# Performance work log

Hardware: AMD Instinct MI355X
Metric: run time of the kernel (lower is better)

Reference implementation:

```python
import jax, jax.numpy as jnp
import numpy as np

N_HEAD = 16

def rel_shift(x):
    # x: (qlen, klen, B, n). Pad one zero column at front of klen axis,
    # reinterpret as (klen+1, qlen, B, n), drop first row, reshape back.
    qlen, klen, b, n = x.shape
    x_pad = jnp.pad(x, ((0, 0), (1, 0), (0, 0), (0, 0)))
    x_pad = x_pad.reshape(klen + 1, qlen, b, n)
    return x_pad[1:].reshape(qlen, klen, b, n)

def setup_inputs() -> dict:
    key = jax.random.key(0)
    ks = jax.random.split(key, 9)
    qlen = klen = 1024
    B = 4
    d_model = 1024
    d_head = d_model // N_HEAD
    q = jax.random.normal(ks[0], (qlen, B, d_model), jnp.float32)
    K = jax.random.normal(ks[1], (klen, B, d_model), jnp.float32)
    V = jax.random.normal(ks[2], (klen, B, d_model), jnp.float32)
    mask = jax.random.bernoulli(ks[3], 0.1, (1, klen, B, 1))
    r = jax.random.normal(ks[4], (klen, d_model), jnp.float32)
    u = jax.random.normal(ks[5], (N_HEAD, d_head), jnp.float32) * 0.02
    v = jax.random.normal(ks[6], (N_HEAD, d_head), jnp.float32) * 0.02
    Wr = jax.random.normal(ks[7], (d_model, d_model), jnp.float32) / np.sqrt(d_model)
    br = jax.random.normal(ks[8], (d_model,), jnp.float32) * 0.02
    return {"q": q, "K": K, "V": V, "mask": mask, "r": r, "u": u, "v": v, "Wr": Wr, "br": br}

def reference(q, K, V, mask, r, u, v, Wr, br):
    qlen, bsz, d_model = q.shape
    klen = K.shape[0]
    d_head = d_model // N_HEAD
    qh = q.reshape(qlen, bsz, N_HEAD, d_head)
    Kh = K.reshape(klen, bsz, N_HEAD, d_head)
    Vh = V.reshape(klen, bsz, N_HEAD, d_head)
    rh = (r @ Wr.T + br).reshape(klen, N_HEAD, d_head)  # r_net projection
    AC = jnp.einsum('ibnd,jbnd->ijbn', qh + u, Kh)
    BD = rel_shift(jnp.einsum('ibnd,jnd->ijbn', qh + v, rh))
    score = (AC + BD) / jnp.sqrt(jnp.asarray(d_head, q.dtype))
    # mask (1,klen,B,1) broadcasts over qlen and heads (torch repeats over heads)
    score = jnp.where(mask, jnp.asarray(-1e9, score.dtype), score)
    weight = jax.nn.softmax(score, axis=1)
    out = jnp.einsum('ijbn,jbnd->ibnd', weight, Vh).reshape(qlen, bsz, d_model)
    return out, weight.mean(axis=-1)
```

## Files before the change

kernel.cpp:

```cpp
#include <hip/hip_runtime.h>
#include <hip/hip_fp16.h>
#include <stdint.h>


#define L 1024
#define BATCH 4
#define NH 16
#define DH 64
#define DM 1024
#define TI 16
#define NJT 16
#define BDP_ST 1032
#define SCALE 0.125f

typedef __attribute__((ext_vector_type(8))) short short8;
typedef __attribute__((ext_vector_type(4))) float f32x4;

static __device__ __forceinline__ unsigned short f2bf(float f) {
    union { float f; unsigned int u; } x; x.f = f;
    return (unsigned short)((x.u + 0x7fffu + ((x.u >> 16) & 1u)) >> 16);
}
static __device__ __forceinline__ float bf2f(unsigned short h) {
    union { unsigned int u; float f; } x; x.u = ((unsigned int)h) << 16;
    return x.f;
}
static __device__ __forceinline__ unsigned short f2h(float f) {
    __half h = __float2half(f);
    union { __half h; unsigned short s; } x; x.h = h; return x.s;
}
static __device__ __forceinline__ float h2f(unsigned short s) {
    union { __half h; unsigned short s; } x; x.s = s; return __half2float(x.h);
}
static __device__ __forceinline__ unsigned short* usp(void* base, int byteoff) {
    return (unsigned short*)((char*)base + byteoff);
}
static __device__ __forceinline__ short8 ld8(const void* base, int byteoff) {
    return *(const short8*)((const char*)base + byteoff);
}
#define SW128(row, colByte) ((((row) * 128) + (colByte)) ^ (((row) & 7) << 4))

__global__ __launch_bounds__(256) void rh_gemm_kernel(
    const float* __restrict__ r, const float* __restrict__ Wr,
    const float* __restrict__ br, float* __restrict__ rhf,
    unsigned short* __restrict__ rhb, int bfmode)
{
    __shared__ float As[16][65];
    __shared__ float Bs[16][65];
    const int j0 = blockIdx.x * 64;
    const int m0 = blockIdx.y * 64;
    const int tid = threadIdx.x;
    const int ty = tid >> 4, tx = tid & 15;
    float acc[4][4] = {};

    for (int k0 = 0; k0 < DM; k0 += 16) {
        const int row = tid >> 2, c4 = (tid & 3) << 2;
        float4 av = *(const float4*)(r  + (size_t)(j0 + row) * DM + k0 + c4);
        float4 bv = *(const float4*)(Wr + (size_t)(m0 + row) * DM + k0 + c4);
        __syncthreads();
        As[c4 + 0][row] = av.x; As[c4 + 1][row] = av.y;
        As[c4 + 2][row] = av.z; As[c4 + 3][row] = av.w;
        Bs[c4 + 0][row] = bv.x; Bs[c4 + 1][row] = bv.y;
        Bs[c4 + 2][row] = bv.z; Bs[c4 + 3][row] = bv.w;
        __syncthreads();
#pragma unroll
        for (int k = 0; k < 16; ++k) {
            float a[4], bb[4];
#pragma unroll
            for (int t = 0; t < 4; ++t) { a[t] = As[k][ty * 4 + t]; bb[t] = Bs[k][tx * 4 + t]; }
#pragma unroll
            for (int ii = 0; ii < 4; ++ii)
#pragma unroll
                for (int jj = 0; jj < 4; ++jj)
                    acc[ii][jj] = fmaf(a[ii], bb[jj], acc[ii][jj]);
        }
    }
#pragma unroll
    for (int ii = 0; ii < 4; ++ii) {
        const int row = j0 + ty * 4 + ii;
#pragma unroll
        for (int jj = 0; jj < 4; ++jj) {
            const int col = m0 + tx * 4 + jj;
            const float val = acc[ii][jj] + br[col];
            if (bfmode)
                rhb[(((size_t)(col >> 6)) * L + row) * DH + (col & 63)] = f2bf(val);
            else
                rhf[(size_t)row * DM + col] = val;
        }
    }
}

__global__ __launch_bounds__(256) void prepass_kernel(
    const float* __restrict__ Kg, const float* __restrict__ Vg,
    unsigned short* __restrict__ Kbf, unsigned short* __restrict__ Vtb)
{
    __shared__ unsigned short tile[64][80];
    const int j0 = blockIdx.x * 64;
    const int b = blockIdx.y, n = blockIdx.z;
    const int bn = b * NH + n;
    const int tid = threadIdx.x;

    for (int idx = tid; idx < 64 * 16; idx += 256) {
        const int jr = idx >> 4, s4 = (idx & 15) * 4;
        const size_t src = ((size_t)(j0 + jr) * BATCH + b) * DM + n * DH + s4;
        float4 kv = *(const float4*)(Kg + src);
        ushort4 o;
        o.x = f2bf(kv.x); o.y = f2bf(kv.y); o.z = f2bf(kv.z); o.w = f2bf(kv.w);
        *(ushort4*)(Kbf + ((size_t)bn * L + j0 + jr) * DH + s4) = o;
        float4 vv4 = *(const float4*)(Vg + src);
        tile[s4 + 0][jr] = f2bf(vv4.x); tile[s4 + 1][jr] = f2bf(vv4.y);
        tile[s4 + 2][jr] = f2bf(vv4.z); tile[s4 + 3][jr] = f2bf(vv4.w);
    }
    __syncthreads();
    for (int idx = tid; idx < 64 * 8; idx += 256) {
        const int d = idx >> 3, p8 = (idx & 7) * 8;
        short8 o = *(const short8*)&tile[d][p8];
        *(short8*)(Vtb + ((size_t)bn * DH + d) * L + j0 + p8) = o;
    }
}

__global__ __launch_bounds__(256) void wm_reduce_kernel(
    const unsigned short* __restrict__ W_ws, float* __restrict__ wm_out)
{
    const int gi = blockIdx.x;
    const int b  = blockIdx.y;
    const int j0 = threadIdx.x * 4;
    float acc0 = 0.f, acc1 = 0.f, acc2 = 0.f, acc3 = 0.f;
#pragma unroll
    for (int n = 0; n < NH; ++n) {
        ushort4 wv = *(const ushort4*)(W_ws + (((size_t)(b * NH + n) * L + gi) * L) + j0);
        acc0 += bf2f(wv.x); acc1 += bf2f(wv.y);
        acc2 += bf2f(wv.z); acc3 += bf2f(wv.w);
    }
    const size_t o = ((size_t)gi * L + j0) * BATCH + b;
    wm_out[o]             = acc0 * (1.f / 16.f);
    wm_out[o + BATCH]     = acc1 * (1.f / 16.f);
    wm_out[o + 2 * BATCH] = acc2 * (1.f / 16.f);
    wm_out[o + 3 * BATCH] = acc3 * (1.f / 16.f);
}

template<int MODE, int PLAIN>
__global__ __launch_bounds__(256, 2) void attn_kernel(
    const float* __restrict__ q,
    const void* __restrict__ Kp, const void* __restrict__ Vp,
    const unsigned char* __restrict__ maskp,
    const float* __restrict__ uu, const float* __restrict__ vvp,
    const void* __restrict__ rhp,
    float* __restrict__ out, float* __restrict__ wm_out,
    unsigned short* __restrict__ W_ws)
{
    __shared__ unsigned short QU[16 * 64];
    __shared__ unsigned short QV[17 * 64];
    __shared__ unsigned short KR[(MODE == 1) ? 64 * 64 : 8];
    __shared__ unsigned short VT[(MODE == 1) ? 64 * 64 : 8];
    __shared__ unsigned short BDp[17 * BDP_ST];
    __shared__ unsigned short Wt[16 * 64];
    __shared__ unsigned char mblk[L];
    __shared__ float denomP[4][16];
    __shared__ float rdenom[16];
    __shared__ int mflags;

    const int i0 = blockIdx.x * TI;
    const int b  = blockIdx.y;
    const int n  = blockIdx.z;
    const int bn = b * NH + n;
    const int tid = threadIdx.x;
    const int w = tid >> 6, lane = tid & 63, lr = lane & 15, lg = lane >> 4;

    const unsigned short* Kbf = (const unsigned short*)Kp;
    const unsigned short* Vtb = (const unsigned short*)Vp;
    const unsigned short* rhb = (const unsigned short*)rhp;
    const float* Kg  = (const float*)Kp;
    const float* Vg  = (const float*)Vp;
    const float* rhf = (const float*)rhp;

    if (tid == 0) mflags = 0;
    __syncthreads();
    {
        int local = 0;
        for (int ww = tid; ww < 1024; ww += 256) {
            const unsigned int word = ((const unsigned int*)maskp)[ww];
            if (word == 0x3f800000u) local |= 1;
            else if (word & 0xffffff00u) local |= 2;
        }
        if (local) atomicOr(&mflags, local);
    }
    __syncthreads();
    {
        const int mtype = (mflags & 1) ? 2 : ((mflags & 2) ? 1 : 0);
        for (int j = tid; j < L; j += 256) {
            bool mv;
            if (mtype == 2)      mv = ((const float*)maskp)[j * BATCH + b] != 0.f;
            else if (mtype == 1) mv = maskp[j * BATCH + b] != 0;
            else                 mv = ((const int*)maskp)[j * BATCH + b] != 0;
            mblk[j] = mv ? 1 : 0;
        }
    }
    for (int idx = tid; idx < 17 * 64; idx += 256) {
        const int row = idx >> 6, d = idx & 63;
        const int gi = i0 + row;
        const float qval = (gi < L) ? q[((size_t)gi * BATCH + b) * DM + n * DH + d] : 0.f;
        *usp(QV, SW128(row, d * 2)) = f2bf(qval + vvp[n * DH + d]);
        if (row < 16) *usp(QU, SW128(row, d * 2)) = f2bf(qval + uu[n * DH + d]);
    }
    __syncthreads();

    for (int ct = 0; ct < 16; ++ct) {
        const int c0 = ct * 64;
        if constexpr (MODE == 1) {
            __syncthreads();
            for (int idx = tid; idx < 64 * 16; idx += 256) {
                const int cr = idx >> 4, d4 = (idx & 15) * 4;
                float4 rv = *(const float4*)(rhf + (size_t)(c0 + cr) * DM + n * DH + d4);
                unsigned short* p = usp(KR, SW128(cr, d4 * 2));
                p[0] = f2bf(rv.x); p[1] = f2bf(rv.y); p[2] = f2bf(rv.z); p[3] = f2bf(rv.w);
            }
            __syncthreads();
        }
        const int ccol = w * 16 + lr;
        f32x4 acc = {0.f, 0.f, 0.f, 0.f};
#pragma unroll
        for (int kh = 0; kh < 2; ++kh) {
            short8 a = ld8(QV, SW128(lr, (kh * 32 + lg * 8) * 2));
            short8 bb;
            if constexpr (MODE == 0)
                bb = *(const short8*)(rhb + ((size_t)n * L + c0 + ccol) * DH + kh * 32 + lg * 8);
            else
                bb = ld8(KR, SW128(ccol, (kh * 32 + lg * 8) * 2));
            acc = __builtin_amdgcn_mfma_f32_16x16x32_bf16(a, bb, acc, 0, 0, 0);
        }
#pragma unroll
        for (int r2 = 0; r2 < 4; ++r2)
            BDp[(lg * 4 + r2) * BDP_ST + c0 + ccol] = f2h(acc[r2]);
        {
            const int col = tid >> 2, kq = (tid & 3) * 16;
            float s16 = 0.f;
#pragma unroll
            for (int kk = 0; kk < 16; kk += 8) {
                short8 qa = ld8(QV, SW128(16, (kq + kk) * 2));
                short8 ra;
                if constexpr (MODE == 0)
                    ra = *(const short8*)(rhb + ((size_t)n * L + c0 + col) * DH + kq + kk);
                else
                    ra = ld8(KR, SW128(col, (kq + kk) * 2));
#pragma unroll
                for (int e = 0; e < 8; ++e)
                    s16 = fmaf(bf2f((unsigned short)qa[e]), bf2f((unsigned short)ra[e]), s16);
            }
            s16 += __shfl_xor(s16, 1);
            s16 += __shfl_xor(s16, 2);
            if ((tid & 3) == 0) BDp[16 * BDP_ST + c0 + col] = f2h(s16);
        }
    }
    __syncthreads();

    f32x4 pv = {0.f, 0.f, 0.f, 0.f};
    float dl[4] = {0.f, 0.f, 0.f, 0.f};
    float tmp[4][NJT];
    const int jloc = w * 16 + lr;
#pragma unroll
    for (int jt = 0; jt < NJT; ++jt) {
        const int j0 = jt * 64;
        const int gj = j0 + jloc;
        if constexpr (MODE == 1) {
            for (int idx = tid; idx < 64 * 16; idx += 256) {
                const int jr = idx >> 4, d4 = (idx & 15) * 4;
                const size_t src = ((size_t)(j0 + jr) * BATCH + b) * DM + n * DH + d4;
                float4 kv = *(const float4*)(Kg + src);
                unsigned short* p = usp(KR, SW128(jr, d4 * 2));
                p[0] = f2bf(kv.x); p[1] = f2bf(kv.y); p[2] = f2bf(kv.z); p[3] = f2bf(kv.w);
                float4 vv4 = *(const float4*)(Vg + src);
                *usp(VT, SW128(d4 + 0, jr * 2)) = f2bf(vv4.x);
                *usp(VT, SW128(d4 + 1, jr * 2)) = f2bf(vv4.y);
                *usp(VT, SW128(d4 + 2, jr * 2)) = f2bf(vv4.z);
                *usp(VT, SW128(d4 + 3, jr * 2)) = f2bf(vv4.w);
            }
            __syncthreads();
        }
        f32x4 acc = {0.f, 0.f, 0.f, 0.f};
#pragma unroll
        for (int kh = 0; kh < 2; ++kh) {
            short8 a = ld8(QU, SW128(lr, (kh * 32 + lg * 8) * 2));
            short8 bb;
            if constexpr (MODE == 0)
                bb = *(const short8*)(Kbf + ((size_t)bn * L + gj) * DH + kh * 32 + lg * 8);
            else
                bb = ld8(KR, SW128(jloc, (kh * 32 + lg * 8) * 2));
            acc = __builtin_amdgcn_mfma_f32_16x16x32_bf16(a, bb, acc, 0, 0, 0);
        }
        const bool msk = mblk[gj] != 0;
#pragma unroll
        for (int r2 = 0; r2 < 4; ++r2) {
            const int il = lg * 4 + r2;
            const int gi = i0 + il;
            const int t = gj - gi;
            float bd = 0.f;
            if (t != 1) {
                const int c = (t <= 0) ? (L - 1 + t) : (t - 2);
                bd = h2f(BDp[(il + (t >= 1 ? 1 : 0)) * BDP_ST + c]);
            }
            float s = (acc[r2] + bd) * SCALE;
            if (msk) s = -1e9f;
            const float wgt = __expf(fminf(s, 80.f));
            dl[r2] += wgt;
            tmp[r2][jt] = wgt;
            *usp(Wt, SW128(il, jloc * 2)) = f2bf(wgt);
        }
        __syncthreads();
#pragma unroll
        for (int kh = 0; kh < 2; ++kh) {
            short8 a = ld8(Wt, SW128(lr, (kh * 32 + lg * 8) * 2));
            short8 bb;
            if constexpr (MODE == 0)
                bb = *(const short8*)(Vtb + ((size_t)bn * DH + jloc) * L + j0 + kh * 32 + lg * 8);
            else
                bb = ld8(VT, SW128(jloc, (kh * 32 + lg * 8) * 2));
            pv = __builtin_amdgcn_mfma_f32_16x16x32_bf16(a, bb, pv, 0, 0, 0);
        }
        __syncthreads();
    }

#pragma unroll
    for (int r2 = 0; r2 < 4; ++r2) {
        float d = dl[r2];
        d += __shfl_xor(d, 1); d += __shfl_xor(d, 2);
        d += __shfl_xor(d, 4); d += __shfl_xor(d, 8);
        if (lr == 0) denomP[w][lg * 4 + r2] = d;
    }
    __syncthreads();
    if (tid < 16)
        rdenom[tid] = 1.f / (denomP[0][tid] + denomP[1][tid] + denomP[2][tid] + denomP[3][tid]);
    __syncthreads();

#pragma unroll
    for (int r2 = 0; r2 < 4; ++r2) {
        const int il = lg * 4 + r2;
        out[((size_t)(i0 + il) * BATCH + b) * DM + n * DH + w * 16 + lr] = pv[r2] * rdenom[il];
    }

    if constexpr (PLAIN == 1) {
#pragma unroll
        for (int r2 = 0; r2 < 4; ++r2) {
            const int il = lg * 4 + r2;
            const float rs = rdenom[il];
            const size_t rowo = ((size_t)bn * L + i0 + il) * L;
#pragma unroll
            for (int jt = 0; jt < NJT; ++jt)
                W_ws[rowo + jt * 64 + jloc] = f2bf(tmp[r2][jt] * rs);
        }
    } else {
#pragma unroll
        for (int r2 = 0; r2 < 4; ++r2) {
            const int il = lg * 4 + r2;
            const float rs = rdenom[il] * (1.f / 16.f);
#pragma unroll
            for (int jt = 0; jt < NJT; ++jt)
                atomicAdd(wm_out + ((size_t)(i0 + il) * L + jt * 64 + jloc) * BATCH + b,
                          tmp[r2][jt] * rs);
        }
    }
}

extern "C" void kernel_launch(void* const* d_in, const int* in_sizes, int n_in,
                              void* d_out, int out_size, void* d_ws, size_t ws_size,
                              hipStream_t stream)
{
    (void)in_sizes; (void)n_in; (void)out_size;
    const float* q   = (const float*)d_in[0];
    const float* K   = (const float*)d_in[1];
    const float* V   = (const float*)d_in[2];
    const unsigned char* mask = (const unsigned char*)d_in[3];
    const float* r   = (const float*)d_in[4];
    const float* u   = (const float*)d_in[5];
    const float* v   = (const float*)d_in[6];
    const float* Wr  = (const float*)d_in[7];
    const float* br  = (const float*)d_in[8];

    float* out = (float*)d_out;
    float* wm  = out + (size_t)L * BATCH * DM;

    const size_t kvbytes = (size_t)BATCH * NH * L * DH * 2;
    const size_t rhbytes = (size_t)NH * L * DH * 2;
    const size_t wmbytes = (size_t)BATCH * NH * L * L * 2;

    if (ws_size >= 2 * kvbytes + rhbytes + wmbytes) {
        unsigned short* Kbf = (unsigned short*)d_ws;
        unsigned short* Vtb = Kbf + kvbytes / 2;
        unsigned short* rhb = Vtb + kvbytes / 2;
        unsigned short* Wws = rhb + rhbytes / 2;
        rh_gemm_kernel<<<dim3(16, 16), 256, 0, stream>>>(r, Wr, br, nullptr, rhb, 1);
        prepass_kernel<<<dim3(16, 4, 16), 256, 0, stream>>>(K, V, Kbf, Vtb);
        attn_kernel<0, 1><<<dim3(64, 4, 16), 256, 0, stream>>>(
            q, Kbf, Vtb, mask, u, v, rhb, out, wm, Wws);
        wm_reduce_kernel<<<dim3(L, BATCH), 256, 0, stream>>>(Wws, wm);
    } else if (ws_size >= 2 * kvbytes + rhbytes) {
        hipMemsetAsync(wm, 0, (size_t)L * L * BATCH * sizeof(float), stream);
        unsigned short* Kbf = (unsigned short*)d_ws;
        unsigned short* Vtb = Kbf + kvbytes / 2;
        unsigned short* rhb = Vtb + kvbytes / 2;
        rh_gemm_kernel<<<dim3(16, 16), 256, 0, stream>>>(r, Wr, br, nullptr, rhb, 1);
        prepass_kernel<<<dim3(16, 4, 16), 256, 0, stream>>>(K, V, Kbf, Vtb);
        attn_kernel<0, 0><<<dim3(64, 4, 16), 256, 0, stream>>>(
            q, Kbf, Vtb, mask, u, v, rhb, out, wm, nullptr);
    } else {
        hipMemsetAsync(wm, 0, (size_t)L * L * BATCH * sizeof(float), stream);
        float* rhf = (float*)d_ws;
        rh_gemm_kernel<<<dim3(16, 16), 256, 0, stream>>>(r, Wr, br, rhf, nullptr, 0);
        attn_kernel<1, 0><<<dim3(64, 4, 16), 256, 0, stream>>>(
            q, K, V, mask, u, v, rhf, out, wm, nullptr);
    }
}
```

Before: 356.6 us.

## Rewrite attention path with MFMA r-projection, exp2 softmax, and streamed weight writes

Replaces the scalar FP32 r_net GEMM with a bf16 MFMA kernel. The main attention kernel is reworked: Q+u/Q+v operands are kept in registers and pre-scaled by log2(e)/sqrt(d), and K/R/V fragments are prefetched from global memory with double buffering. Softmax uses exp2 without max subtraction, and per-wave PV accumulation runs over 256-key slabs without block-wide syncs. Unnormalized bf16 weights go straight to the workspace, and the reduction kernel applies per-row reciprocal denominators. Occupancy is raised to 3 blocks per CU; the trade-offs are bf16 rounding of r_net and the loss of overflow safety from skipping max subtraction.

```diff
diff --git a/kernel.cpp b/kernel.cpp
--- a/kernel.cpp
+++ b/kernel.cpp
@@ -12,6 +12,7 @@
 #define NJT 16
 #define BDP_ST 1032
 #define SCALE 0.125f
+#define CS 0.18033688011112042f
 
 typedef __attribute__((ext_vector_type(8))) short short8;
 typedef __attribute__((ext_vector_type(4))) float f32x4;
@@ -37,12 +38,63 @@
 static __device__ __forceinline__ short8 ld8(const void* base, int byteoff) {
     return *(const short8*)((const char*)base + byteoff);
 }
+static __device__ __forceinline__ float fexp2(float x) {
+#if __has_builtin(__builtin_amdgcn_exp2f)
+    return __builtin_amdgcn_exp2f(x);
+#else
+    return __expf(x * 0.6931471805599453f);
+#endif
+}
 #define SW128(row, colByte) ((((row) * 128) + (colByte)) ^ (((row) & 7) << 4))
+
+__global__ __launch_bounds__(256) void rh_gemm_mfma(
+    const float* __restrict__ r, const float* __restrict__ Wr,
+    const float* __restrict__ br, unsigned short* __restrict__ rhb)
+{
+    __shared__ unsigned short rT[64 * 64];
+    __shared__ unsigned short wT[64 * 64];
+    const int c0 = blockIdx.x * 64, m0 = blockIdx.y * 64;
+    const int tid = threadIdx.x;
+    const int w = tid >> 6, lane = tid & 63, lr = lane & 15, lg = lane >> 4;
+    f32x4 acc[4] = {};
+
+    for (int kt = 0; kt < 16; ++kt) {
+        const int k0 = kt * 64;
+        __syncthreads();
+        const int row = tid >> 2, cb = (tid & 3) * 16;
+#pragma unroll
+        for (int q4 = 0; q4 < 4; ++q4) {
+            float4 rv = *(const float4*)(r + (size_t)(c0 + row) * DM + k0 + cb + q4 * 4);
+            unsigned short* p = usp(rT, SW128(row, (cb + q4 * 4) * 2));
+            p[0] = f2bf(rv.x); p[1] = f2bf(rv.y); p[2] = f2bf(rv.z); p[3] = f2bf(rv.w);
+            float4 wv = *(const float4*)(Wr + (size_t)(m0 + row) * DM + k0 + cb + q4 * 4);
+            unsigned short* pw = usp(wT, SW128(row, (cb + q4 * 4) * 2));
+            pw[0] = f2bf(wv.x); pw[1] = f2bf(wv.y); pw[2] = f2bf(wv.z); pw[3] = f2bf(wv.w);
+        }
+        __syncthreads();
+#pragma unroll
+        for (int mch = 0; mch < 4; ++mch)
+#pragma unroll
+            for (int kh = 0; kh < 2; ++kh) {
+                short8 a  = ld8(rT, SW128(w * 16 + lr,   (kh * 32 + lg * 8) * 2));
+                short8 bb = ld8(wT, SW128(mch * 16 + lr, (kh * 32 + lg * 8) * 2));
+                acc[mch] = __builtin_amdgcn_mfma_f32_16x16x32_bf16(a, bb, acc[mch], 0, 0, 0);
+            }
+    }
+#pragma unroll
+    for (int mch = 0; mch < 4; ++mch)
+#pragma unroll
+        for (int r2 = 0; r2 < 4; ++r2) {
+            const int c = c0 + w * 16 + lg * 4 + r2;
+            const int d = mch * 16 + lr;
+            const float val = acc[mch][r2] + br[m0 + d];
+            rhb[((size_t)blockIdx.y * L + c) * DH + d] = f2bf(val);
+        }
+}
 
 __global__ __launch_bounds__(256) void rh_gemm_kernel(
     const float* __restrict__ r, const float* __restrict__ Wr,
-    const float* __restrict__ br, float* __restrict__ rhf,
-    unsigned short* __restrict__ rhb, int bfmode)
+    const float* __restrict__ br, float* __restrict__ rhf)
 {
     __shared__ float As[16][65];
     __shared__ float Bs[16][65];
@@ -80,11 +132,7 @@
 #pragma unroll
         for (int jj = 0; jj < 4; ++jj) {
             const int col = m0 + tx * 4 + jj;
-            const float val = acc[ii][jj] + br[col];
-            if (bfmode)
-                rhb[(((size_t)(col >> 6)) * L + row) * DH + (col & 63)] = f2bf(val);
-            else
-                rhf[(size_t)row * DM + col] = val;
+            rhf[(size_t)row * DM + col] = acc[ii][jj] + br[col];
         }
     }
 }
@@ -119,41 +167,39 @@
 }
 
 __global__ __launch_bounds__(256) void wm_reduce_kernel(
-    const unsigned short* __restrict__ W_ws, float* __restrict__ wm_out)
+    const unsigned short* __restrict__ W_ws, const float* __restrict__ rdeng,
+    float* __restrict__ wm_out)
 {
     const int gi = blockIdx.x;
     const int b  = blockIdx.y;
     const int j0 = threadIdx.x * 4;
-    float acc0 = 0.f, acc1 = 0.f, acc2 = 0.f, acc3 = 0.f;
+    float a0 = 0.f, a1 = 0.f, a2 = 0.f, a3 = 0.f;
 #pragma unroll
     for (int n = 0; n < NH; ++n) {
-        ushort4 wv = *(const ushort4*)(W_ws + (((size_t)(b * NH + n) * L + gi) * L) + j0);
-        acc0 += bf2f(wv.x); acc1 += bf2f(wv.y);
-        acc2 += bf2f(wv.z); acc3 += bf2f(wv.w);
+        const int bn = b * NH + n;
+        const float rd = rdeng[((size_t)bn << 10) + gi];
+        ushort4 wv = *(const ushort4*)(W_ws + ((size_t)bn * L + gi) * L + j0);
+        a0 += bf2f(wv.x) * rd; a1 += bf2f(wv.y) * rd;
+        a2 += bf2f(wv.z) * rd; a3 += bf2f(wv.w) * rd;
     }
     const size_t o = ((size_t)gi * L + j0) * BATCH + b;
-    wm_out[o]             = acc0 * (1.f / 16.f);
-    wm_out[o + BATCH]     = acc1 * (1.f / 16.f);
-    wm_out[o + 2 * BATCH] = acc2 * (1.f / 16.f);
-    wm_out[o + 3 * BATCH] = acc3 * (1.f / 16.f);
-}
-
-template<int MODE, int PLAIN>
-__global__ __launch_bounds__(256, 2) void attn_kernel(
+    wm_out[o]             = a0;
+    wm_out[o + BATCH]     = a1;
+    wm_out[o + 2 * BATCH] = a2;
+    wm_out[o + 3 * BATCH] = a3;
+}
+
+__global__ __launch_bounds__(256, 3) void attn_fused(
     const float* __restrict__ q,
-    const void* __restrict__ Kp, const void* __restrict__ Vp,
+    const unsigned short* __restrict__ Kbf, const unsigned short* __restrict__ Vtb,
     const unsigned char* __restrict__ maskp,
     const float* __restrict__ uu, const float* __restrict__ vvp,
-    const void* __restrict__ rhp,
-    float* __restrict__ out, float* __restrict__ wm_out,
-    unsigned short* __restrict__ W_ws)
+    const unsigned short* __restrict__ rhb,
+    float* __restrict__ out, unsigned short* __restrict__ W_ws,
+    float* __restrict__ rdeng)
 {
-    __shared__ unsigned short QU[16 * 64];
-    __shared__ unsigned short QV[17 * 64];
-    __shared__ unsigned short KR[(MODE == 1) ? 64 * 64 : 8];
-    __shared__ unsigned short VT[(MODE == 1) ? 64 * 64 : 8];
-    __shared__ unsigned short BDp[17 * BDP_ST];
-    __shared__ unsigned short Wt[16 * 64];
+    __shared__ __align__(16) unsigned short BDp[17 * BDP_ST];
+    __shared__ __align__(16) unsigned short Wt[4][2][16 * 64];
     __shared__ unsigned char mblk[L];
     __shared__ float denomP[4][16];
     __shared__ float rdenom[16];
@@ -165,13 +211,6 @@
     const int bn = b * NH + n;
     const int tid = threadIdx.x;
     const int w = tid >> 6, lane = tid & 63, lr = lane & 15, lg = lane >> 4;
-
-    const unsigned short* Kbf = (const unsigned short*)Kp;
-    const unsigned short* Vtb = (const unsigned short*)Vp;
-    const unsigned short* rhb = (const unsigned short*)rhp;
-    const float* Kg  = (const float*)Kp;
-    const float* Vg  = (const float*)Vp;
-    const float* rhf = (const float*)rhp;
 
     if (tid == 0) mflags = 0;
     __syncthreads();
@@ -195,17 +234,264 @@
             mblk[j] = mv ? 1 : 0;
         }
     }
+    if (tid < 17 * 8) {
+        const int row = tid >> 3, cp = tid & 7;
+        BDp[row * BDP_ST + 1024 + cp] = 0;
+    }
+
+    const float* qrow = q + ((size_t)(i0 + lr) * BATCH + b) * DM + n * DH;
+    const float* urow = uu + n * DH;
+    const float* vrow = vvp + n * DH;
+    short8 qu_a[2], qv_a[2];
+#pragma unroll
+    for (int kh = 0; kh < 2; ++kh) {
+        const int kb = kh * 32 + lg * 8;
+        float4 qa = *(const float4*)(qrow + kb), qb = *(const float4*)(qrow + kb + 4);
+        float4 ua = *(const float4*)(urow + kb), ub = *(const float4*)(urow + kb + 4);
+        float4 va = *(const float4*)(vrow + kb), vb = *(const float4*)(vrow + kb + 4);
+        short8 su, sv;
+        su[0] = (short)f2bf((qa.x + ua.x) * CS); su[1] = (short)f2bf((qa.y + ua.y) * CS);
+        su[2] = (short)f2bf((qa.z + ua.z) * CS); su[3] = (short)f2bf((qa.w + ua.w) * CS);
+        su[4] = (short)f2bf((qb.x + ub.x) * CS); su[5] = (short)f2bf((qb.y + ub.y) * CS);
+        su[6] = (short)f2bf((qb.z + ub.z) * CS); su[7] = (short)f2bf((qb.w + ub.w) * CS);
+        sv[0] = (short)f2bf((qa.x + va.x) * CS); sv[1] = (short)f2bf((qa.y + va.y) * CS);
+        sv[2] = (short)f2bf((qa.z + va.z) * CS); sv[3] = (short)f2bf((qa.w + va.w) * CS);
+        sv[4] = (short)f2bf((qb.x + vb.x) * CS); sv[5] = (short)f2bf((qb.y + vb.y) * CS);
+        sv[6] = (short)f2bf((qb.z + vb.z) * CS); sv[7] = (short)f2bf((qb.w + vb.w) * CS);
+        qu_a[kh] = su; qv_a[kh] = sv;
+    }
+    float qv16[16];
+    {
+        const int kq = (tid & 3) * 16;
+        if (i0 + 16 < L) {
+            const float* q16 = q + ((size_t)(i0 + 16) * BATCH + b) * DM + n * DH;
+#pragma unroll
+            for (int e4 = 0; e4 < 4; ++e4) {
+                float4 qa = *(const float4*)(q16 + kq + e4 * 4);
+                float4 va = *(const float4*)(vrow + kq + e4 * 4);
+                qv16[e4 * 4 + 0] = (qa.x + va.x) * CS; qv16[e4 * 4 + 1] = (qa.y + va.y) * CS;
+                qv16[e4 * 4 + 2] = (qa.z + va.z) * CS; qv16[e4 * 4 + 3] = (qa.w + va.w) * CS;
+            }
+        } else {
+#pragma unroll
+            for (int e = 0; e < 16; ++e) qv16[e] = 0.f;
+        }
+    }
+
+    {
+        const unsigned short* rpane = rhb + (size_t)n * L * DH;
+        const int ccol = w * 16 + lr;
+        short8 rb[2][2];
+#pragma unroll
+        for (int kh = 0; kh < 2; ++kh)
+            rb[0][kh] = *(const short8*)(rpane + (size_t)ccol * DH + kh * 32 + lg * 8);
+        const int col16 = tid >> 2;
+        const int kq = (tid & 3) * 16;
+#pragma unroll
+        for (int ct = 0; ct < 16; ++ct) {
+            const int c0 = ct * 64;
+            const int cur = ct & 1;
+            if (ct + 1 < 16) {
+#pragma unroll
+                for (int kh = 0; kh < 2; ++kh)
+                    rb[cur ^ 1][kh] = *(const short8*)(rpane + (size_t)((ct + 1) * 64 + ccol) * DH + kh * 32 + lg * 8);
+            }
+            f32x4 acc = {0.f, 0.f, 0.f, 0.f};
+#pragma unroll
+            for (int kh = 0; kh < 2; ++kh)
+                acc = __builtin_amdgcn_mfma_f32_16x16x32_bf16(qv_a[kh], rb[cur][kh], acc, 0, 0, 0);
+#pragma unroll
+            for (int r2 = 0; r2 < 4; ++r2)
+                BDp[(lg * 4 + r2) * BDP_ST + c0 + ccol] = f2h(acc[r2]);
+            {
+                short8 ra0 = *(const short8*)(rpane + (size_t)(c0 + col16) * DH + kq);
+                short8 ra1 = *(const short8*)(rpane + (size_t)(c0 + col16) * DH + kq + 8);
+                float s16 = 0.f;
+#pragma unroll
+                for (int e = 0; e < 8; ++e) {
+                    s16 = fmaf(qv16[e],     bf2f((unsigned short)ra0[e]), s16);
+                    s16 = fmaf(qv16[e + 8], bf2f((unsigned short)ra1[e]), s16);
+                }
+                s16 += __shfl_xor(s16, 1);
+                s16 += __shfl_xor(s16, 2);
+                if ((tid & 3) == 0) BDp[16 * BDP_ST + c0 + col16] = f2h(s16);
+            }
+        }
+    }
+    __syncthreads();
+
+    const unsigned short* Kpane = Kbf + (size_t)bn * L * DH;
+    const unsigned short* Vpane = Vtb + (size_t)bn * DH * L;
+    const int jwbase = w * 256;
+    f32x4 pv[4] = {};
+    float dl[4] = {0.f, 0.f, 0.f, 0.f};
+    int ilb[4];
+    size_t wsrow[4];
+#pragma unroll
+    for (int r2 = 0; r2 < 4; ++r2) {
+        ilb[r2] = (lg * 4 + r2) * BDP_ST;
+        wsrow[r2] = ((size_t)bn * L + i0 + lg * 4 + r2) * L;
+    }
+    short8 kf[2][2];
+#pragma unroll
+    for (int kh = 0; kh < 2; ++kh)
+        kf[0][kh] = *(const short8*)(Kpane + (size_t)(jwbase + lr) * DH + kh * 32 + lg * 8);
+
+#pragma unroll 1
+    for (int sub = 0; sub < 4; ++sub) {
+        const int jbase = jwbase + sub * 64;
+        unsigned short* WtW = &Wt[w][sub & 1][0];
+        short8 vfr[8];
+#pragma unroll
+        for (int dch = 0; dch < 4; ++dch)
+#pragma unroll
+            for (int kh = 0; kh < 2; ++kh)
+                vfr[dch * 2 + kh] = *(const short8*)(Vpane + (size_t)(dch * 16 + lr) * L + jbase + kh * 32 + lg * 8);
+#pragma unroll
+        for (int c4 = 0; c4 < 4; ++c4) {
+            const int chunk = sub * 4 + c4;
+            const int cur = c4 & 1;
+            if (chunk + 1 < 16) {
+#pragma unroll
+                for (int kh = 0; kh < 2; ++kh)
+                    kf[cur ^ 1][kh] = *(const short8*)(Kpane + (size_t)(jwbase + (chunk + 1) * 16 + lr) * DH + kh * 32 + lg * 8);
+            }
+            f32x4 acc = {0.f, 0.f, 0.f, 0.f};
+#pragma unroll
+            for (int kh = 0; kh < 2; ++kh)
+                acc = __builtin_amdgcn_mfma_f32_16x16x32_bf16(qu_a[kh], kf[cur][kh], acc, 0, 0, 0);
+            const int gj = jbase + c4 * 16 + lr;
+            const float mo = mblk[gj] ? -1e9f : 0.f;
+            const int ebase = gj - i0 - lg * 4;
+#pragma unroll
+            for (int r2 = 0; r2 < 4; ++r2) {
+                const int e = ebase - r2;
+                const int addr = ilb[r2] + e + ((e <= 0) ? 1023 : 1030);
+                const float bd = h2f(BDp[addr]);
+                float s = fminf(acc[r2] + bd + mo, 126.f);
+                const float wg = fexp2(s);
+                dl[r2] += wg;
+                const unsigned short wb = f2bf(wg);
+                *usp(WtW, SW128(lg * 4 + r2, (c4 * 16 + lr) * 2)) = wb;
+                W_ws[wsrow[r2] + gj] = wb;
+            }
+        }
+#pragma unroll
+        for (int dch = 0; dch < 4; ++dch)
+#pragma unroll
+            for (int kh = 0; kh < 2; ++kh) {
+                short8 a = ld8(WtW, SW128(lr, (kh * 32 + lg * 8) * 2));
+                pv[dch] = __builtin_amdgcn_mfma_f32_16x16x32_bf16(a, vfr[dch * 2 + kh], pv[dch], 0, 0, 0);
+            }
+    }
+
+#pragma unroll
+    for (int r2 = 0; r2 < 4; ++r2) {
+        float d = dl[r2];
+        d += __shfl_xor(d, 1); d += __shfl_xor(d, 2);
+        d += __shfl_xor(d, 4); d += __shfl_xor(d, 8);
+        if (lr == 0) denomP[w][lg * 4 + r2] = d;
+    }
+    {
+        float* pvw = (float*)&Wt[w][0][0];
+#pragma unroll
+        for (int dch = 0; dch < 4; ++dch)
+#pragma unroll
+            for (int r2 = 0; r2 < 4; ++r2)
+                pvw[(lg * 4 + r2) * 64 + dch * 16 + lr] = pv[dch][r2];
+    }
+    __syncthreads();
+    if (tid < 16) {
+        const float dn = denomP[0][tid] + denomP[1][tid] + denomP[2][tid] + denomP[3][tid];
+        rdenom[tid] = 1.f / dn;
+        rdeng[((size_t)bn << 10) + i0 + tid] = 1.f / (dn * 16.f);
+    }
+    __syncthreads();
+
+    {
+        const float* pvwAll = (const float*)&Wt[0][0][0];
+        const int il = tid >> 4, d0 = (tid & 15) * 4;
+        float4 o = *(const float4*)(pvwAll + 0 * 1024 + il * 64 + d0);
+        float4 o1 = *(const float4*)(pvwAll + 1 * 1024 + il * 64 + d0);
+        float4 o2 = *(const float4*)(pvwAll + 2 * 1024 + il * 64 + d0);
+        float4 o3 = *(const float4*)(pvwAll + 3 * 1024 + il * 64 + d0);
+        const float rs = rdenom[il];
+        o.x = (o.x + o1.x + o2.x + o3.x) * rs;
+        o.y = (o.y + o1.y + o2.y + o3.y) * rs;
+        o.z = (o.z + o1.z + o2.z + o3.z) * rs;
+        o.w = (o.w + o1.w + o2.w + o3.w) * rs;
+        *(float4*)(out + ((size_t)(i0 + il) * BATCH + b) * DM + n * DH + d0) = o;
+    }
+}
+
+template<int MODE>
+__global__ __launch_bounds__(256, 2) void attn_legacy(
+    const float* __restrict__ q,
+    const void* __restrict__ Kp, const void* __restrict__ Vp,
+    const unsigned char* __restrict__ maskp,
+    const float* __restrict__ uu, const float* __restrict__ vvp,
+    const void* __restrict__ rhp,
+    float* __restrict__ out, float* __restrict__ wm_out)
+{
+    __shared__ unsigned short QU[16 * 64];
+    __shared__ unsigned short QV[17 * 64];
+    __shared__ unsigned short KR[(MODE == 1) ? 64 * 64 : 8];
+    __shared__ unsigned short VT[(MODE == 1) ? 64 * 64 : 8];
+    __shared__ unsigned short BDp[17 * BDP_ST];
+    __shared__ unsigned short Wt[2][16 * 64];
+    __shared__ unsigned char mblk[L];
+    __shared__ float denomP[4][16];
+    __shared__ float rdenom[16];
+    __shared__ int mflags;
+
+    const int i0 = blockIdx.x * TI;
+    const int b  = blockIdx.y;
+    const int n  = blockIdx.z;
+    const int bn = b * NH + n;
+    const int tid = threadIdx.x;
+    const int w = tid >> 6, lane = tid & 63, lr = lane & 15, lg = lane >> 4;
+
+    const unsigned short* Kbf = (const unsigned short*)Kp;
+    const unsigned short* Vtb = (const unsigned short*)Vp;
+    const unsigned short* rhb = (const unsigned short*)rhp;
+    const float* Kg  = (const float*)Kp;
+    const float* Vg  = (const float*)Vp;
+    const float* rhf = (const float*)rhp;
+
+    if (tid == 0) mflags = 0;
+    __syncthreads();
+    {
+        int local = 0;
+        for (int ww = tid; ww < 1024; ww += 256) {
+            const unsigned int word = ((const unsigned int*)maskp)[ww];
+            if (word == 0x3f800000u) local |= 1;
+            else if (word & 0xffffff00u) local |= 2;
+        }
+        if (local) atomicOr(&mflags, local);
+    }
+    __syncthreads();
+    {
+        const int mtype = (mflags & 1) ? 2 : ((mflags & 2) ? 1 : 0);
+        for (int j = tid; j < L; j += 256) {
+            bool mv;
+            if (mtype == 2)      mv = ((const float*)maskp)[j * BATCH + b] != 0.f;
+            else if (mtype == 1) mv = maskp[j * BATCH + b] != 0;
+            else                 mv = ((const int*)maskp)[j * BATCH + b] != 0;
+            mblk[j] = mv ? 1 : 0;
+        }
+    }
     for (int idx = tid; idx < 17 * 64; idx += 256) {
         const int row = idx >> 6, d = idx & 63;
         const int gi = i0 + row;
         const float qval = (gi < L) ? q[((size_t)gi * BATCH + b) * DM + n * DH + d] : 0.f;
-        *usp(QV, SW128(row, d * 2)) = f2bf(qval + vvp[n * DH + d]);
-        if (row < 16) *usp(QU, SW128(row, d * 2)) = f2bf(qval + uu[n * DH + d]);
+        *usp(QV, SW128(row, d * 2)) = f2bf((qval + vvp[n * DH + d]) * SCALE);
+        if (row < 16) *usp(QU, SW128(row, d * 2)) = f2bf((qval + uu[n * DH + d]) * SCALE);
     }
     __syncthreads();
 
     for (int ct = 0; ct < 16; ++ct) {
         const int c0 = ct * 64;
+        const int ccol = w * 16 + lr;
         if constexpr (MODE == 1) {
             __syncthreads();
             for (int idx = tid; idx < 64 * 16; idx += 256) {
@@ -216,7 +502,6 @@
             }
             __syncthreads();
         }
-        const int ccol = w * 16 + lr;
         f32x4 acc = {0.f, 0.f, 0.f, 0.f};
 #pragma unroll
         for (int kh = 0; kh < 2; ++kh) {
@@ -251,17 +536,20 @@
             if ((tid & 3) == 0) BDp[16 * BDP_ST + c0 + col] = f2h(s16);
         }
     }
+
+    const int jloc = w * 16 + lr;
     __syncthreads();
 
     f32x4 pv = {0.f, 0.f, 0.f, 0.f};
     float dl[4] = {0.f, 0.f, 0.f, 0.f};
     float tmp[4][NJT];
-    const int jloc = w * 16 + lr;
 #pragma unroll
     for (int jt = 0; jt < NJT; ++jt) {
         const int j0 = jt * 64;
         const int gj = j0 + jloc;
+        const int cur = jt & 1;
         if constexpr (MODE == 1) {
+            __syncthreads();
             for (int idx = tid; idx < 64 * 16; idx += 256) {
                 const int jr = idx >> 4, d4 = (idx & 15) * 4;
                 const size_t src = ((size_t)(j0 + jr) * BATCH + b) * DM + n * DH + d4;
@@ -298,17 +586,17 @@
                 const int c = (t <= 0) ? (L - 1 + t) : (t - 2);
                 bd = h2f(BDp[(il + (t >= 1 ? 1 : 0)) * BDP_ST + c]);
             }
-            float s = (acc[r2] + bd) * SCALE;
+            float s = acc[r2] + bd;
             if (msk) s = -1e9f;
             const float wgt = __expf(fminf(s, 80.f));
             dl[r2] += wgt;
             tmp[r2][jt] = wgt;
-            *usp(Wt, SW128(il, jloc * 2)) = f2bf(wgt);
+            *usp(Wt[cur], SW128(il, jloc * 2)) = f2bf(wgt);
         }
         __syncthreads();
 #pragma unroll
         for (int kh = 0; kh < 2; ++kh) {
-            short8 a = ld8(Wt, SW128(lr, (kh * 32 + lg * 8) * 2));
+            short8 a = ld8(Wt[cur], SW128(lr, (kh * 32 + lg * 8) * 2));
             short8 bb;
             if constexpr (MODE == 0)
                 bb = *(const short8*)(Vtb + ((size_t)bn * DH + jloc) * L + j0 + kh * 32 + lg * 8);
@@ -316,7 +604,6 @@
                 bb = ld8(VT, SW128(jloc, (kh * 32 + lg * 8) * 2));
             pv = __builtin_amdgcn_mfma_f32_16x16x32_bf16(a, bb, pv, 0, 0, 0);
         }
-        __syncthreads();
     }
 
 #pragma unroll
@@ -336,27 +623,14 @@
         const int il = lg * 4 + r2;
         out[((size_t)(i0 + il) * BATCH + b) * DM + n * DH + w * 16 + lr] = pv[r2] * rdenom[il];
     }
-
-    if constexpr (PLAIN == 1) {
-#pragma unroll
-        for (int r2 = 0; r2 < 4; ++r2) {
-            const int il = lg * 4 + r2;
-            const float rs = rdenom[il];
-            const size_t rowo = ((size_t)bn * L + i0 + il) * L;
-#pragma unroll
-            for (int jt = 0; jt < NJT; ++jt)
-                W_ws[rowo + jt * 64 + jloc] = f2bf(tmp[r2][jt] * rs);
-        }
-    } else {
-#pragma unroll
-        for (int r2 = 0; r2 < 4; ++r2) {
-            const int il = lg * 4 + r2;
-            const float rs = rdenom[il] * (1.f / 16.f);
-#pragma unroll
-            for (int jt = 0; jt < NJT; ++jt)
-                atomicAdd(wm_out + ((size_t)(i0 + il) * L + jt * 64 + jloc) * BATCH + b,
-                          tmp[r2][jt] * rs);
-        }
+#pragma unroll
+    for (int r2 = 0; r2 < 4; ++r2) {
+        const int il = lg * 4 + r2;
+        const float rs = rdenom[il] * (1.f / 16.f);
+#pragma unroll
+        for (int jt = 0; jt < NJT; ++jt)
+            atomicAdd(wm_out + ((size_t)(i0 + il) * L + jt * 64 + jloc) * BATCH + b,
+                      tmp[r2][jt] * rs);
     }
 }
 
@@ -381,31 +655,33 @@
     const size_t kvbytes = (size_t)BATCH * NH * L * DH * 2;
     const size_t rhbytes = (size_t)NH * L * DH * 2;
     const size_t wmbytes = (size_t)BATCH * NH * L * L * 2;
-
-    if (ws_size >= 2 * kvbytes + rhbytes + wmbytes) {
+    const size_t rdbytes = (size_t)BATCH * NH * L * 4;
+
+    if (ws_size >= 2 * kvbytes + rhbytes + wmbytes + rdbytes) {
         unsigned short* Kbf = (unsigned short*)d_ws;
         unsigned short* Vtb = Kbf + kvbytes / 2;
         unsigned short* rhb = Vtb + kvbytes / 2;
         unsigned short* Wws = rhb + rhbytes / 2;
-        rh_gemm_kernel<<<dim3(16, 16), 256, 0, stream>>>(r, Wr, br, nullptr, rhb, 1);
+        float* rdeng = (float*)(Wws + wmbytes / 2);
+        rh_gemm_mfma<<<dim3(16, 16), 256, 0, stream>>>(r, Wr, br, rhb);
         prepass_kernel<<<dim3(16, 4, 16), 256, 0, stream>>>(K, V, Kbf, Vtb);
-        attn_kernel<0, 1><<<dim3(64, 4, 16), 256, 0, stream>>>(
-            q, Kbf, Vtb, mask, u, v, rhb, out, wm, Wws);
-        wm_reduce_kernel<<<dim3(L, BATCH), 256, 0, stream>>>(Wws, wm);
+        attn_fused<<<dim3(64, 4, 16), 256, 0, stream>>>(
+            q, Kbf, Vtb, mask, u, v, rhb, out, Wws, rdeng);
+        wm_reduce_kernel<<<dim3(L, BATCH), 256, 0, stream>>>(Wws, rdeng, wm);
     } else if (ws_size >= 2 * kvbytes + rhbytes) {
         hipMemsetAsync(wm, 0, (size_t)L * L * BATCH * sizeof(float), stream);
         unsigned short* Kbf = (unsigned short*)d_ws;
         unsigned short* Vtb = Kbf + kvbytes / 2;
         unsigned short* rhb = Vtb + kvbytes / 2;
-        rh_gemm_kernel<<<dim3(16, 16), 256, 0, stream>>>(r, Wr, br, nullptr, rhb, 1);
+        rh_gemm_mfma<<<dim3(16, 16), 256, 0, stream>>>(r, Wr, br, rhb);
         prepass_kernel<<<dim3(16, 4, 16), 256, 0, stream>>>(K, V, Kbf, Vtb);
-        attn_kernel<0, 0><<<dim3(64, 4, 16), 256, 0, stream>>>(
-            q, Kbf, Vtb, mask, u, v, rhb, out, wm, nullptr);
+        attn_legacy<0><<<dim3(64, 4, 16), 256, 0, stream>>>(
+            q, Kbf, Vtb, mask, u, v, rhb, out, wm);
     } else {
         hipMemsetAsync(wm, 0, (size_t)L * L * BATCH * sizeof(float), stream);
         float* rhf = (float*)d_ws;
-        rh_gemm_kernel<<<dim3(16, 16), 256, 0, stream>>>(r, Wr, br, rhf, nullptr, 0);
-        attn_kernel<1, 0><<<dim3(64, 4, 16), 256, 0, stream>>>(
-            q, K, V, mask, u, v, rhf, out, wm, nullptr);
-    }
-}
+        rh_gemm_kernel<<<dim3(16, 16), 256, 0, stream>>>(r, Wr, br, rhf);
+        attn_legacy<1><<<dim3(64, 4, 16), 256, 0, stream>>>(
+            q, K, V, mask, u, v, rhf, out, wm);
+    }
+}
```

Result: faster. 297.2 us (-16.7%).
